# Kernel tuning notes

Hardware: AMD Instinct MI355X
Metric: run time of the kernel (lower is better)

Reference implementation:

```python
import jax, jax.numpy as jnp
import numpy as np

B, N, D = 8, 2048, 256

def setup_inputs() -> dict:
    key = jax.random.key(0)
    ks = jax.random.split(key, 8)
    sc = 1.0 / np.sqrt(D)
    return {
        "x": jax.random.normal(ks[0], (B, N, D), dtype=jnp.float32),
        "W_fp": jax.random.normal(ks[1], (D, D), dtype=jnp.float32) * sc,
        "b_fp": jnp.zeros((D,), dtype=jnp.float32),
        "w_s": jax.random.normal(ks[2], (D,), dtype=jnp.float32) * sc,
        "b_s": jnp.zeros((), dtype=jnp.float32),
        "W_rp": jax.random.normal(ks[3], (D, D), dtype=jnp.float32) * sc,
        "b_rp": jnp.zeros((D,), dtype=jnp.float32),
        "W_gp": jax.random.normal(ks[4], (D, D), dtype=jnp.float32) * sc,
        "b_gp": jnp.zeros((D,), dtype=jnp.float32),
        "gamma": jnp.ones((D,), dtype=jnp.float32),
        "beta": jnp.zeros((D,), dtype=jnp.float32),
    }

def reference(x, W_fp, b_fp, w_s, b_s, W_rp, b_rp, W_gp, b_gp, gamma, beta):
    # feature projection: [B, N, D]
    proj = jnp.einsum('bnd,de->bne', x, W_fp) + b_fp
    # F.normalize(p=2, dim=-1) with eps=1e-12
    nrm = jnp.sqrt(jnp.sum(proj * proj, axis=-1, keepdims=True))
    xn = proj / jnp.maximum(nrm, 1e-12)
    # cosine similarity matrix [B, N, N]
    sim = jnp.einsum('bnd,bmd->bnm', xn, xn)
    # adj_scaler: Linear(D,1)+sigmoid is constant along the broadcast axis ->
    # compute per-node scalar once [B, N] (same math as the O(N^2*D) expand)
    s = jax.nn.sigmoid(jnp.einsum('bnd,d->bn', proj, w_s) + b_s)
    scaler = jnp.clip(0.5 * (s[:, :, None] + s[:, None, :]), 1e-6, 1.0)
    adj = jnp.maximum(scaler * sim, 1e-6)  # clamp(min=1e-6)
    degree = jnp.maximum(jnp.sum(adj, axis=2, keepdims=True), 1e-6)
    norm_adj = adj / degree
    # aggregation + region projection
    region = jnp.einsum('bnm,bmd->bnd', norm_adj, proj)
    region = jnp.einsum('bnd,de->bne', region, W_rp) + b_rp
    # global pooling + projection: [B, 1, D]
    g = jnp.mean(region, axis=1, keepdims=True)
    g = jnp.einsum('bnd,de->bne', g, W_gp) + b_gp
    input_global = jnp.mean(x, axis=1, keepdims=True)
    h = g + input_global
    # LayerNorm (eps=1e-5)
    mu = jnp.mean(h, axis=-1, keepdims=True)
    var = jnp.mean((h - mu) ** 2, axis=-1, keepdims=True)
    out = (h - mu) / jnp.sqrt(var + 1e-5) * gamma + beta
    return out, adj
```

## Files before the change

kernel.cpp:

```cpp
#include <hip/hip_runtime.h>
#include <hip/hip_bf16.h>
#include <math.h>

#define Bn 8
#define Nn 2048
#define Dn 256

typedef short short8 __attribute__((ext_vector_type(8)));
typedef float floatx4 __attribute__((ext_vector_type(4)));

__device__ __forceinline__ short f2bf_bits(float f) {
    __bf16 h = (__bf16)f;
    return __builtin_bit_cast(short, h);
}

__device__ __forceinline__ float bf2f(short s) {
    unsigned u = ((unsigned)(unsigned short)s) << 16;
    return __builtin_bit_cast(float, u);
}

__device__ __forceinline__ void gl_lds16(const void* gsrc, void* ldst) {
    __builtin_amdgcn_global_load_lds(
        (const __attribute__((address_space(1))) void*)gsrc,
        (__attribute__((address_space(3))) void*)ldst, 16, 0, 0);
}

__device__ __forceinline__ float sigmoidf_(float z) {
    return 1.0f / (1.0f + __expf(-z));
}


__global__ void k_transpose(const float* __restrict__ W, short* __restrict__ Wt) {
    int e = blockIdx.x, d = threadIdx.x;
    Wt[e * Dn + d] = f2bf_bits(W[d * Dn + e]);
}


__global__ __launch_bounds__(256) void k_projxn(
    const float* __restrict__ x, const short* __restrict__ Wt,
    const float* __restrict__ b_fp, const float* __restrict__ w_s,
    short* __restrict__ xn, float* __restrict__ sdot, float* __restrict__ nrm,
    float* __restrict__ xpart) {
    __shared__ __align__(16) short As[64 * 64];
    __shared__ __align__(16) short Bs[256 * 64];
    __shared__ float xsumS[4 * 256];
    const int t = threadIdx.x;
    const int bm = blockIdx.x * 64;
    const int lane = t & 63, wv = t >> 6;
    const int wm = wv * 16;
    const int l15 = lane & 15, q = lane >> 4;

    for (int i = t; i < 1024; i += 256) xsumS[i] = 0.f;

    floatx4 acc[16];
    #pragma unroll
    for (int j = 0; j < 16; ++j) acc[j] = (floatx4){0.f, 0.f, 0.f, 0.f};

    const int rA = t >> 2, cA = (t & 3) * 16;
    const int rB = t >> 3, cB = (t & 7) * 8;

    for (int k0 = 0; k0 < Dn; k0 += 64) {
        const float* gp = x + (size_t)(bm + rA) * Dn + k0 + cA;
        float4 v0 = *(const float4*)gp;
        float4 v1 = *(const float4*)(gp + 4);
        float4 v2 = *(const float4*)(gp + 8);
        float4 v3 = *(const float4*)(gp + 12);
        short8 o0, o1;
        o0[0] = f2bf_bits(v0.x); o0[1] = f2bf_bits(v0.y);
        o0[2] = f2bf_bits(v0.z); o0[3] = f2bf_bits(v0.w);
        o0[4] = f2bf_bits(v1.x); o0[5] = f2bf_bits(v1.y);
        o0[6] = f2bf_bits(v1.z); o0[7] = f2bf_bits(v1.w);
        o1[0] = f2bf_bits(v2.x); o1[1] = f2bf_bits(v2.y);
        o1[2] = f2bf_bits(v2.z); o1[3] = f2bf_bits(v2.w);
        o1[4] = f2bf_bits(v3.x); o1[5] = f2bf_bits(v3.y);
        o1[6] = f2bf_bits(v3.z); o1[7] = f2bf_bits(v3.w);
        *(short8*)(As + rA * 64 + cA) = o0;
        *(short8*)(As + rA * 64 + cA + 8) = o1;
        #pragma unroll
        for (int cc = 0; cc < 8; ++cc)
            gl_lds16(Wt + (size_t)(cc * 32 + rB) * Dn + k0 + cB,
                     Bs + (cc * 32 + rB) * 64 + cB);
        __syncthreads();
        #pragma unroll
        for (int ks = 0; ks < 2; ++ks) {
            short8 af = *(const short8*)(As + (wm + l15) * 64 + ks * 32 + q * 8);
            #pragma unroll
            for (int j = 0; j < 16; ++j) {
                short8 bfr = *(const short8*)(Bs + (j * 16 + l15) * 64 + ks * 32 + q * 8);
                acc[j] = __builtin_amdgcn_mfma_f32_16x16x32_bf16(af, bfr, acc[j], 0, 0, 0);
            }
        }
        {
            float s = 0.f;
            #pragma unroll
            for (int r = 0; r < 16; ++r)
                s += bf2f(As[(wm + r) * 64 + lane]);
            xsumS[wv * 256 + k0 + lane] += s;
        }
        __syncthreads();
    }
    {
        float xs = xsumS[t] + xsumS[256 + t] + xsumS[512 + t] + xsumS[768 + t];
        xpart[(size_t)blockIdx.x * Dn + t] = xs;
    }
    float bfv[16], wsv[16];
    #pragma unroll
    for (int j = 0; j < 16; ++j) {
        bfv[j] = b_fp[j * 16 + l15];
        wsv[j] = w_s[j * 16 + l15];
    }
    #pragma unroll
    for (int reg = 0; reg < 4; ++reg) {
        int row = bm + wm + q * 4 + reg;
        float v[16];
        float pw = 0.f, pn = 0.f;
        #pragma unroll
        for (int j = 0; j < 16; ++j) {
            v[j] = acc[j][reg] + bfv[j];
            pw += v[j] * wsv[j];
            pn += v[j] * v[j];
        }
        #pragma unroll
        for (int m = 1; m < 16; m <<= 1) {
            pw += __shfl_xor(pw, m);
            pn += __shfl_xor(pn, m);
        }
        float nc = fmaxf(sqrtf(pn), 1e-12f);
        float inv = 1.0f / nc;
        size_t rbase = (size_t)row * Dn + l15;
        #pragma unroll
        for (int j = 0; j < 16; ++j)
            xn[rbase + j * 16] = f2bf_bits(v[j] * inv);
        if (l15 == 0) {
            sdot[row] = pw;
            nrm[row] = nc;
        }
    }
}


__global__ __launch_bounds__(256) void k_sim(
    const short* __restrict__ xn, const float* __restrict__ sdot,
    const float* __restrict__ b_s, float* __restrict__ adj,
    float* __restrict__ deg_part) {
    __shared__ __align__(16) short As[128 * 64];
    __shared__ __align__(16) short Bs[128 * 64];
    __shared__ float degS[2][128];
    const int t = threadIdx.x;
    const int cx = blockIdx.x;
    const int bn = cx * 128;
    const int bm = blockIdx.y * 128;
    const int b = blockIdx.z;
    const int lane = t & 63, wv = t >> 6;
    const int wm = (wv >> 1) * 64, wn = (wv & 1) * 64;
    const int l15 = lane & 15, q = lane >> 4;
    const int rr = t >> 3, c8 = (t & 7) * 8;
    const short* xb = xn + (size_t)b * Nn * Dn;

    floatx4 acc[4][4];
    #pragma unroll
    for (int i = 0; i < 4; ++i)
        #pragma unroll
        for (int j = 0; j < 4; ++j) acc[i][j] = (floatx4){0.f, 0.f, 0.f, 0.f};

    for (int k0 = 0; k0 < Dn; k0 += 64) {
        #pragma unroll
        for (int cc = 0; cc < 4; ++cc) {
            int r = cc * 32 + rr;
            gl_lds16(xb + (size_t)(bm + r) * Dn + k0 + c8, As + r * 64 + c8);
            gl_lds16(xb + (size_t)(bn + r) * Dn + k0 + c8, Bs + r * 64 + c8);
        }
        __syncthreads();
        #pragma unroll
        for (int ks = 0; ks < 2; ++ks) {
            short8 af[4], bfr[4];
            #pragma unroll
            for (int i = 0; i < 4; ++i)
                af[i] = *(const short8*)(As + (wm + i * 16 + l15) * 64 + ks * 32 + q * 8);
            #pragma unroll
            for (int j = 0; j < 4; ++j)
                bfr[j] = *(const short8*)(Bs + (wn + j * 16 + l15) * 64 + ks * 32 + q * 8);
            #pragma unroll
            for (int i = 0; i < 4; ++i)
                #pragma unroll
                for (int j = 0; j < 4; ++j)
                    acc[i][j] = __builtin_amdgcn_mfma_f32_16x16x32_bf16(af[i], bfr[j], acc[i][j], 0, 0, 0);
        }
        __syncthreads();
    }
    const float bsv = b_s[0];
    float scol[4];
    #pragma unroll
    for (int j = 0; j < 4; ++j)
        scol[j] = sigmoidf_(sdot[b * Nn + bn + wn + j * 16 + l15] + bsv);
    #pragma unroll
    for (int i = 0; i < 4; ++i) {
        #pragma unroll
        for (int reg = 0; reg < 4; ++reg) {
            int lr = wm + i * 16 + q * 4 + reg;
            int row = bm + lr;
            float srow = sigmoidf_(sdot[b * Nn + row] + bsv);
            size_t obase = ((size_t)b * Nn + row) * Nn + bn + wn + l15;
            float rs = 0.f;
            #pragma unroll
            for (int j = 0; j < 4; ++j) {
                float sc = 0.5f * (srow + scol[j]);
                sc = fminf(fmaxf(sc, 1e-6f), 1.0f);
                float v = fmaxf(sc * acc[i][j][reg], 1e-6f);
                adj[obase + (size_t)j * 16] = v;
                rs += v;
            }
            #pragma unroll
            for (int m = 1; m < 16; m <<= 1) rs += __shfl_xor(rs, m);
            if (l15 == 0) degS[wv & 1][lr] = rs;
        }
    }
    __syncthreads();
    if (t < 128)
        deg_part[((size_t)(b * 16 + cx)) * Nn + bm + t] = degS[0][t] + degS[1][t];
}


__global__ __launch_bounds__(512) void k_colsum(
    const float* __restrict__ adj, const float* __restrict__ deg_part,
    const short* __restrict__ xn, const float* __restrict__ nrm,
    float* __restrict__ gpart) {
    int b = blockIdx.x, ck = blockIdx.y, t = threadIdx.x;
    __shared__ float invdeg[Nn];
    __shared__ float part[32][64];
    __shared__ float csL[64];
    #pragma unroll
    for (int rc = 0; rc < 4; ++rc) {
        int row = rc * 512 + t;
        float s = 0.f;
        #pragma unroll
        for (int cx = 0; cx < 16; ++cx)
            s += deg_part[((size_t)(b * 16 + cx)) * Nn + row];
        invdeg[row] = 1.0f / fmaxf(s, 1e-6f);
    }
    __syncthreads();
    const int lc = (t & 15) * 4;
    const int rg = t >> 4;
    const int c0 = ck * 64;
    float sx = 0.f, sy = 0.f, sz = 0.f, sw = 0.f;
    for (int r = rg; r < Nn; r += 32) {
        float4 v = *(const float4*)(adj + ((size_t)b * Nn + r) * Nn + c0 + lc);
        float w = invdeg[r];
        sx += v.x * w; sy += v.y * w; sz += v.z * w; sw += v.w * w;
    }
    part[rg][lc + 0] = sx; part[rg][lc + 1] = sy;
    part[rg][lc + 2] = sz; part[rg][lc + 3] = sw;
    __syncthreads();
    if (t < 64) {
        float s = 0.f;
        #pragma unroll
        for (int g = 0; g < 32; ++g) s += part[g][t];
        csL[t] = s * nrm[b * Nn + c0 + t];
    }
    __syncthreads();
    if (t < Dn) {
        float g = 0.f;
        #pragma unroll 4
        for (int m = 0; m < 64; ++m)
            g += csL[m] * bf2f(xn[((size_t)(b * Nn + c0 + m)) * Dn + t]);
        gpart[(b * 32 + ck) * Dn + t] = g;
    }
}


__global__ __launch_bounds__(256) void k_final2(
    const float* __restrict__ gpart, const float* __restrict__ xpart,
    const float* __restrict__ W_rp, const float* __restrict__ b_rp,
    const float* __restrict__ W_gp, const float* __restrict__ b_gp,
    const float* __restrict__ gamma, const float* __restrict__ beta,
    float* __restrict__ out) {
    int b = blockIdx.x, t = threadIdx.x;
    __shared__ float gp_s[Dn];
    __shared__ float g1_s[Dn];
    __shared__ float red[8];
    float gs = 0.f, xs = 0.f;
    #pragma unroll
    for (int ck = 0; ck < 32; ++ck) {
        gs += gpart[(b * 32 + ck) * Dn + t];
        xs += xpart[(b * 32 + ck) * Dn + t];
    }
    gp_s[t] = gs * (1.0f / Nn);
    float xm = xs * (1.0f / Nn);
    __syncthreads();
    float g1 = b_rp[t];
    #pragma unroll 4
    for (int d = 0; d < Dn; ++d) g1 += gp_s[d] * W_rp[d * Dn + t];
    g1_s[t] = g1;
    __syncthreads();
    float g2 = b_gp[t];
    #pragma unroll 4
    for (int e = 0; e < Dn; ++e) g2 += g1_s[e] * W_gp[e * Dn + t];
    float h = g2 + xm;
    float sum = h;
    #pragma unroll
    for (int m = 1; m < 64; m <<= 1) sum += __shfl_xor(sum, m);
    if ((t & 63) == 0) red[t >> 6] = sum;
    __syncthreads();
    float mu = (red[0] + red[1] + red[2] + red[3]) * (1.0f / Dn);
    float dv = h - mu;
    float s2 = dv * dv;
    #pragma unroll
    for (int m = 1; m < 64; m <<= 1) s2 += __shfl_xor(s2, m);
    if ((t & 63) == 0) red[4 + (t >> 6)] = s2;
    __syncthreads();
    float var = (red[4] + red[5] + red[6] + red[7]) * (1.0f / Dn);
    out[b * Dn + t] = dv * rsqrtf(var + 1e-5f) * gamma[t] + beta[t];
}


extern "C" void kernel_launch(void* const* d_in, const int* in_sizes, int n_in,
                              void* d_out, int out_size, void* d_ws, size_t ws_size,
                              hipStream_t stream) {
    const float* x     = (const float*)d_in[0];
    const float* W_fp  = (const float*)d_in[1];
    const float* b_fp  = (const float*)d_in[2];
    const float* w_s   = (const float*)d_in[3];
    const float* b_s   = (const float*)d_in[4];
    const float* W_rp  = (const float*)d_in[5];
    const float* b_rp  = (const float*)d_in[6];
    const float* W_gp  = (const float*)d_in[7];
    const float* b_gp  = (const float*)d_in[8];
    const float* gamma = (const float*)d_in[9];
    const float* beta  = (const float*)d_in[10];

    float* out = (float*)d_out;
    float* adj = out + Bn * Dn;

    char* ws = (char*)d_ws;
    short* xn    = (short*)(ws);
    short* Wt    = (short*)(ws + 8388608);
    float* sdot  = (float*)(ws + 8519680);
    float* nrm   = (float*)(ws + 8585216);
    float* degp  = (float*)(ws + 8650752);
    float* gpart = (float*)(ws + 9699328);
    float* xpart = (float*)(ws + 9961472);

    k_transpose<<<Dn, Dn, 0, stream>>>(W_fp, Wt);
    k_projxn<<<(Bn * Nn) / 64, 256, 0, stream>>>(x, Wt, b_fp, w_s, xn, sdot, nrm, xpart);
    k_sim<<<dim3(Nn / 128, Nn / 128, Bn), 256, 0, stream>>>(xn, sdot, b_s, adj, degp);
    k_colsum<<<dim3(Bn, 32), 512, 0, stream>>>(adj, degp, xn, nrm, gpart);
    k_final2<<<Bn, 256, 0, stream>>>(gpart, xpart, W_rp, b_rp, W_gp, b_gp, gamma, beta, out);
}
```

Before: 287.7 us.

## Split projection kernel into 16-row blocks with column-split waves

The projection/normalize kernel now processes 16 rows per block instead of 64, launching four times as many blocks. Each wave computes a 64-column slice of those 16 rows, so the per-row squared-norm and score dot products are combined across waves through shared memory before normalizing. The per-block x-sum partials grow from 32 to 128 per batch, and the final kernel's reduction loop is updated to match. The aim is to fill more compute units during the projection, at the cost of reloading the full weight tile into LDS four times as often, plus an extra barrier and reduction.

```diff
diff --git a/kernel.cpp b/kernel.cpp
--- a/kernel.cpp
+++ b/kernel.cpp
@@ -7,6 +7,7 @@
 #define Dn 256
 
 typedef short short8 __attribute__((ext_vector_type(8)));
+typedef short short4v __attribute__((ext_vector_type(4)));
 typedef float floatx4 __attribute__((ext_vector_type(4)));
 
 __device__ __forceinline__ short f2bf_bits(float f) {
@@ -41,41 +42,31 @@
     const float* __restrict__ b_fp, const float* __restrict__ w_s,
     short* __restrict__ xn, float* __restrict__ sdot, float* __restrict__ nrm,
     float* __restrict__ xpart) {
-    __shared__ __align__(16) short As[64 * 64];
+    __shared__ __align__(16) short As[16 * 64];
     __shared__ __align__(16) short Bs[256 * 64];
-    __shared__ float xsumS[4 * 256];
+    __shared__ float xsumS[4][256];
+    __shared__ float pwS[4][16], pnS[4][16];
     const int t = threadIdx.x;
-    const int bm = blockIdx.x * 64;
+    const int bm = blockIdx.x * 16;
     const int lane = t & 63, wv = t >> 6;
-    const int wm = wv * 16;
     const int l15 = lane & 15, q = lane >> 4;
-
-    for (int i = t; i < 1024; i += 256) xsumS[i] = 0.f;
-
-    floatx4 acc[16];
-    #pragma unroll
-    for (int j = 0; j < 16; ++j) acc[j] = (floatx4){0.f, 0.f, 0.f, 0.f};
-
-    const int rA = t >> 2, cA = (t & 3) * 16;
+    const int cw = wv * 64;
+
+    for (int i = t; i < 1024; i += 256) ((float*)xsumS)[i] = 0.f;
+
+    floatx4 acc[4];
+    #pragma unroll
+    for (int j = 0; j < 4; ++j) acc[j] = (floatx4){0.f, 0.f, 0.f, 0.f};
+
+    const int rA = t >> 4, cA = (t & 15) * 4;
     const int rB = t >> 3, cB = (t & 7) * 8;
 
     for (int k0 = 0; k0 < Dn; k0 += 64) {
-        const float* gp = x + (size_t)(bm + rA) * Dn + k0 + cA;
-        float4 v0 = *(const float4*)gp;
-        float4 v1 = *(const float4*)(gp + 4);
-        float4 v2 = *(const float4*)(gp + 8);
-        float4 v3 = *(const float4*)(gp + 12);
-        short8 o0, o1;
-        o0[0] = f2bf_bits(v0.x); o0[1] = f2bf_bits(v0.y);
-        o0[2] = f2bf_bits(v0.z); o0[3] = f2bf_bits(v0.w);
-        o0[4] = f2bf_bits(v1.x); o0[5] = f2bf_bits(v1.y);
-        o0[6] = f2bf_bits(v1.z); o0[7] = f2bf_bits(v1.w);
-        o1[0] = f2bf_bits(v2.x); o1[1] = f2bf_bits(v2.y);
-        o1[2] = f2bf_bits(v2.z); o1[3] = f2bf_bits(v2.w);
-        o1[4] = f2bf_bits(v3.x); o1[5] = f2bf_bits(v3.y);
-        o1[6] = f2bf_bits(v3.z); o1[7] = f2bf_bits(v3.w);
-        *(short8*)(As + rA * 64 + cA) = o0;
-        *(short8*)(As + rA * 64 + cA + 8) = o1;
+        float4 v = *(const float4*)(x + (size_t)(bm + rA) * Dn + k0 + cA);
+        short4v o;
+        o[0] = f2bf_bits(v.x); o[1] = f2bf_bits(v.y);
+        o[2] = f2bf_bits(v.z); o[3] = f2bf_bits(v.w);
+        *(short4v*)(As + rA * 64 + cA) = o;
         #pragma unroll
         for (int cc = 0; cc < 8; ++cc)
             gl_lds16(Wt + (size_t)(cc * 32 + rB) * Dn + k0 + cB,
@@ -83,59 +74,63 @@
         __syncthreads();
         #pragma unroll
         for (int ks = 0; ks < 2; ++ks) {
-            short8 af = *(const short8*)(As + (wm + l15) * 64 + ks * 32 + q * 8);
-            #pragma unroll
-            for (int j = 0; j < 16; ++j) {
-                short8 bfr = *(const short8*)(Bs + (j * 16 + l15) * 64 + ks * 32 + q * 8);
+            short8 af = *(const short8*)(As + l15 * 64 + ks * 32 + q * 8);
+            #pragma unroll
+            for (int j = 0; j < 4; ++j) {
+                short8 bfr = *(const short8*)(Bs + (cw + j * 16 + l15) * 64 + ks * 32 + q * 8);
                 acc[j] = __builtin_amdgcn_mfma_f32_16x16x32_bf16(af, bfr, acc[j], 0, 0, 0);
             }
         }
         {
-            float s = 0.f;
-            #pragma unroll
-            for (int r = 0; r < 16; ++r)
-                s += bf2f(As[(wm + r) * 64 + lane]);
-            xsumS[wv * 256 + k0 + lane] += s;
+            int col = t & 63;
+            float s = bf2f(As[(wv * 4 + 0) * 64 + col]) + bf2f(As[(wv * 4 + 1) * 64 + col])
+                    + bf2f(As[(wv * 4 + 2) * 64 + col]) + bf2f(As[(wv * 4 + 3) * 64 + col]);
+            xsumS[wv][k0 + col] += s;
         }
         __syncthreads();
     }
-    {
-        float xs = xsumS[t] + xsumS[256 + t] + xsumS[512 + t] + xsumS[768 + t];
-        xpart[(size_t)blockIdx.x * Dn + t] = xs;
-    }
-    float bfv[16], wsv[16];
-    #pragma unroll
-    for (int j = 0; j < 16; ++j) {
-        bfv[j] = b_fp[j * 16 + l15];
-        wsv[j] = w_s[j * 16 + l15];
+    float bfv[4], wsv[4], vreg[4][4];
+    #pragma unroll
+    for (int j = 0; j < 4; ++j) {
+        bfv[j] = b_fp[cw + j * 16 + l15];
+        wsv[j] = w_s[cw + j * 16 + l15];
     }
     #pragma unroll
     for (int reg = 0; reg < 4; ++reg) {
-        int row = bm + wm + q * 4 + reg;
-        float v[16];
+        int r = q * 4 + reg;
         float pw = 0.f, pn = 0.f;
         #pragma unroll
-        for (int j = 0; j < 16; ++j) {
-            v[j] = acc[j][reg] + bfv[j];
-            pw += v[j] * wsv[j];
-            pn += v[j] * v[j];
+        for (int j = 0; j < 4; ++j) {
+            float v = acc[j][reg] + bfv[j];
+            vreg[reg][j] = v;
+            pw += v * wsv[j];
+            pn += v * v;
         }
         #pragma unroll
         for (int m = 1; m < 16; m <<= 1) {
             pw += __shfl_xor(pw, m);
             pn += __shfl_xor(pn, m);
         }
+        if (l15 == 0) { pwS[wv][r] = pw; pnS[wv][r] = pn; }
+    }
+    __syncthreads();
+    #pragma unroll
+    for (int reg = 0; reg < 4; ++reg) {
+        int r = q * 4 + reg;
+        float pn = pnS[0][r] + pnS[1][r] + pnS[2][r] + pnS[3][r];
         float nc = fmaxf(sqrtf(pn), 1e-12f);
         float inv = 1.0f / nc;
-        size_t rbase = (size_t)row * Dn + l15;
-        #pragma unroll
-        for (int j = 0; j < 16; ++j)
-            xn[rbase + j * 16] = f2bf_bits(v[j] * inv);
-        if (l15 == 0) {
-            sdot[row] = pw;
-            nrm[row] = nc;
-        }
-    }
+        size_t rbase = (size_t)(bm + r) * Dn + cw + l15;
+        #pragma unroll
+        for (int j = 0; j < 4; ++j)
+            xn[rbase + j * 16] = f2bf_bits(vreg[reg][j] * inv);
+        if (wv == 0 && l15 == 0) {
+            sdot[bm + r] = pwS[0][r] + pwS[1][r] + pwS[2][r] + pwS[3][r];
+            nrm[bm + r] = nc;
+        }
+    }
+    float xs = xsumS[0][t] + xsumS[1][t] + xsumS[2][t] + xsumS[3][t];
+    xpart[(size_t)blockIdx.x * Dn + t] = xs;
 }
 
 
@@ -280,10 +275,11 @@
     __shared__ float red[8];
     float gs = 0.f, xs = 0.f;
     #pragma unroll
-    for (int ck = 0; ck < 32; ++ck) {
+    for (int ck = 0; ck < 32; ++ck)
         gs += gpart[(b * 32 + ck) * Dn + t];
-        xs += xpart[(b * 32 + ck) * Dn + t];
-    }
+    #pragma unroll 4
+    for (int ck = 0; ck < 128; ++ck)
+        xs += xpart[((size_t)b * 128 + ck) * Dn + t];
     gp_s[t] = gs * (1.0f / Nn);
     float xm = xs * (1.0f / Nn);
     __syncthreads();
@@ -341,7 +337,7 @@
     float* xpart = (float*)(ws + 9961472);
 
     k_transpose<<<Dn, Dn, 0, stream>>>(W_fp, Wt);
-    k_projxn<<<(Bn * Nn) / 64, 256, 0, stream>>>(x, Wt, b_fp, w_s, xn, sdot, nrm, xpart);
+    k_projxn<<<(Bn * Nn) / 16, 256, 0, stream>>>(x, Wt, b_fp, w_s, xn, sdot, nrm, xpart);
     k_sim<<<dim3(Nn / 128, Nn / 128, Bn), 256, 0, stream>>>(xn, sdot, b_s, adj, degp);
     k_colsum<<<dim3(Bn, 32), 512, 0, stream>>>(adj, degp, xn, nrm, gpart);
     k_final2<<<Bn, 256, 0, stream>>>(gpart, xpart, W_rp, b_rp, W_gp, b_gp, gamma, beta, out);
```

New measurement: 297.8 us. 3.5% more time.
